# Optimization experiments

Hardware: AMD Instinct MI355X
Metric: run time of the kernel (lower is better)

Reference implementation:

```python
import jax, jax.numpy as jnp
import numpy as np

N = 200_000
E = 3_200_000
H = 24

def setup_inputs() -> dict:
    key = jax.random.key(0)
    ks = jax.random.split(key, 12)
    s = 1.0 / np.sqrt(H).astype(np.float32)
    u = lambda k, shape: jax.random.uniform(k, shape, jnp.float32, -s, s)
    return {
        "x": jax.random.normal(ks[0], (N,), jnp.float32),
        "h0": jax.random.normal(ks[1], (1, N, H), jnp.float32) * 0.1,
        "c0": jax.random.normal(ks[2], (1, N, H), jnp.float32) * 0.1,
        "edge_index": jax.random.randint(ks[3], (2, E), 0, N, dtype=jnp.int32),
        "w_ih": u(ks[4], (4 * H, 1)),
        "w_hh": u(ks[5], (4 * H, H)),
        "b_ih": u(ks[6], (4 * H,)),
        "b_hh": u(ks[7], (4 * H,)),
        "gcn_w": u(ks[8], (H, H)),
        "gcn_b": u(ks[9], (H,)),
        "lin_w": u(ks[10], (1, H)),
        "lin_b": u(ks[11], (1,)),
    }

def reference(x, h0, c0, edge_index, w_ih, w_hh, b_ih, b_hh, gcn_w, gcn_b, lin_w, lin_b):
    # --- LSTM single step (seq_len=1, batch=N, input_size=1, hidden=H) ---
    h_prev = h0[0]  # [N, H]
    c_prev = c0[0]  # [N, H]
    # gates in torch order: input, forget, cell(g), output
    gates = x[:, None] * w_ih[:, 0][None, :] + b_ih + h_prev @ w_hh.T + b_hh  # [N, 4H]
    i, f, g, o = jnp.split(gates, 4, axis=-1)
    i = jax.nn.sigmoid(i); f = jax.nn.sigmoid(f); o = jax.nn.sigmoid(o); g = jnp.tanh(g)
    c = f * c_prev + i * g
    h = o * jnp.tanh(c)  # [N, H] -- LSTM output == new hidden state

    # --- GCNConv(24,24): symmetric norm with self loops (PyG default) ---
    xw = h @ gcn_w.T  # [N, H]
    src, dst = edge_index[0], edge_index[1]
    deg = jax.ops.segment_sum(jnp.ones(src.shape, xw.dtype), dst, num_segments=N) + 1.0
    dinv = jax.lax.rsqrt(deg)                      # deg >= 1 due to self loops
    norm = dinv[src] * dinv[dst]                   # [E]
    msg = xw[src] * norm[:, None]                  # [E, H]
    agg = jax.ops.segment_sum(msg, dst, num_segments=N)
    agg = agg + xw * (dinv * dinv)[:, None]        # self-loop edges
    conv = agg + gcn_b                             # [N, H]

    # --- Linear(24,1) + elementwise gate ---
    out = (conv @ lin_w.T + lin_b).reshape(-1)     # [N]
    return x * out, h[None], c[None]
```

## Files before the change

kernel.cpp:

```cpp
#include <hip/hip_runtime.h>
#include <math.h>

#define H 24
#define B0 4096
#define B0_SHIFT 12
#define MAXNB 64
#define NBPAD 65
#define REP1 8
#define REP3 4
#define P 8
#define CAP 70000
#define CSTRIDE 16
#define K1_EPB 8192
#define EPT (K1_EPB / 256)

__device__ __forceinline__ float sigmoidf_(float v) {
    return 1.0f / (1.0f + __expf(-v));
}
__device__ __forceinline__ float tanhf_(float v) {
    return 1.0f - 2.0f / (__expf(2.0f * v) + 1.0f);
}

__global__ void init_kernel(unsigned* __restrict__ cursors,
                            const float* __restrict__ gcn_w,
                            const float* __restrict__ gcn_b,
                            const float* __restrict__ lin_w,
                            const float* __restrict__ lin_b,
                            float* __restrict__ g, float* __restrict__ cb, int NB) {
    int t = threadIdx.x;
    if (t < H) {
        float acc = 0.0f;
        for (int j = 0; j < H; j++) acc = fmaf(lin_w[j], gcn_w[j * H + t], acc);
        g[t] = acc;
    }
    if (t == 32) {
        float c = lin_b[0];
        for (int j = 0; j < H; j++) c = fmaf(gcn_b[j], lin_w[j], c);
        *cb = c;
    }
    if (t < MAXNB) cursors[t * CSTRIDE] = (unsigned)t * CAP;
}

__global__ __launch_bounds__(256) void scatter_kernel(
    const int* __restrict__ src, const int* __restrict__ dst,
    unsigned* __restrict__ cursors, unsigned* __restrict__ pedge, int E, int NB)
{
    __shared__ unsigned cnt[REP1 * NBPAD];
    __shared__ unsigned rbase[REP3][MAXNB];
    __shared__ unsigned c3[REP3 * NBPAD];
    int start = blockIdx.x * K1_EPB;
    int end   = start + K1_EPB; if (end > E) end = E;
    int rep1 = threadIdx.x & (REP1 - 1);
    int rep3 = rep1 >> 1;

    for (int i = threadIdx.x; i < REP1 * NBPAD; i += 256) cnt[i] = 0;
    __syncthreads();

    unsigned dreg[EPT];
    #pragma unroll
    for (int q = 0; q < EPT; q++) {
        int e = start + q * 256 + threadIdx.x;
        if (e < end) {
            unsigned d = (unsigned)dst[e];
            dreg[q] = d;
            atomicAdd(&cnt[rep1 * NBPAD + (d >> B0_SHIFT)], 1u);
        }
    }
    __syncthreads();

    for (int i = threadIdx.x; i < NB; i += 256) {
        unsigned c[REP1];
        unsigned tot = 0;
        #pragma unroll
        for (int r = 0; r < REP1; r++) { c[r] = cnt[r * NBPAD + i]; tot += c[r]; }
        unsigned gb = tot ? atomicAdd(&cursors[i * CSTRIDE], tot) : 0u;
        unsigned s0 = c[0] + c[1], s1 = c[2] + c[3], s2 = c[4] + c[5];
        rbase[0][i] = gb;
        rbase[1][i] = gb + s0;
        rbase[2][i] = gb + s0 + s1;
        rbase[3][i] = gb + s0 + s1 + s2;
        #pragma unroll
        for (int r = 0; r < REP3; r++) c3[r * NBPAD + i] = 0;
    }
    __syncthreads();

    #pragma unroll
    for (int q = 0; q < EPT; q++) {
        int e = start + q * 256 + threadIdx.x;
        if (e < end) {
            unsigned d = dreg[q];
            unsigned b = d >> B0_SHIFT;
            unsigned slot = atomicAdd(&c3[rep3 * NBPAD + b], 1u);
            unsigned idx  = rbase[rep3][b] + slot;
            if (idx < (b + 1u) * CAP)
                pedge[idx] = ((unsigned)src[e] << B0_SHIFT) | (d & (B0 - 1));
        }
    }
}

__global__ __launch_bounds__(256) void deghist_kernel(
    const unsigned* __restrict__ pedge, const unsigned* __restrict__ cursors,
    unsigned short* __restrict__ degp, int NB, int NPAD)
{
    __shared__ unsigned h[B0];
    int b = blockIdx.x % NB, p = blockIdx.x / NB;
    for (int i = threadIdx.x; i < B0; i += 256) h[i] = 0;
    __syncthreads();
    unsigned base = (unsigned)b * CAP;
    unsigned sz = cursors[b * CSTRIDE] - base; if (sz > CAP) sz = CAP;
    unsigned chunk = (sz + P - 1) / P;
    unsigned s0 = p * chunk;
    unsigned s1 = s0 + chunk; if (s1 > sz) s1 = sz;
    for (unsigned i = s0 + threadIdx.x; i < s1; i += 256)
        atomicAdd(&h[pedge[base + i] & (B0 - 1)], 1u);
    __syncthreads();
    unsigned short* out = degp + (size_t)p * NPAD + (size_t)b * B0;
    for (int i = threadIdx.x; i < B0; i += 256) out[i] = (unsigned short)h[i];
}

__global__ __launch_bounds__(256) void node_kernel(
    const float* __restrict__ x, const float* __restrict__ h0, const float* __restrict__ c0,
    const float* __restrict__ w_ih, const float* __restrict__ w_hh,
    const float* __restrict__ b_ih, const float* __restrict__ b_hh,
    const float* __restrict__ g,
    float* __restrict__ out_h, float* __restrict__ out_c,
    float* __restrict__ y, int N)
{
    __shared__ float ws[96 * 24];
    __shared__ float swih[96];
    __shared__ float sbs[96];
    __shared__ float sg[24];

    #pragma unroll 3
    for (int i = threadIdx.x; i < 96 * 24; i += 256) ws[i] = w_hh[i];
    if (threadIdx.x < 96) {
        swih[threadIdx.x] = w_ih[threadIdx.x];
        sbs[threadIdx.x]  = b_ih[threadIdx.x] + b_hh[threadIdx.x];
    } else if (threadIdx.x >= 128 && threadIdx.x < 152) {
        sg[threadIdx.x - 128] = g[threadIdx.x - 128];
    }
    __syncthreads();

    int tid = blockIdx.x * 256 + threadIdx.x;
    int pr  = tid >> 2;
    int n0  = pr * 2;
    if (n0 >= N) return;
    int n1  = n0 + 1;
    int t   = tid & 3;
    int k0  = 6 * t;

    float hp0[H], hp1[H];
    {
        const float4* a4 = (const float4*)(h0 + (size_t)n0 * H);
        const float4* b4 = (const float4*)(h0 + (size_t)n1 * H);
        #pragma unroll
        for (int q = 0; q < 6; q++) {
            float4 va = a4[q], vb = b4[q];
            hp0[4*q+0] = va.x; hp0[4*q+1] = va.y; hp0[4*q+2] = va.z; hp0[4*q+3] = va.w;
            hp1[4*q+0] = vb.x; hp1[4*q+1] = vb.y; hp1[4*q+2] = vb.z; hp1[4*q+3] = vb.w;
        }
    }
    float cp0[6], cp1[6];
    {
        const float2* a2 = (const float2*)(c0 + (size_t)n0 * H + k0);
        const float2* b2 = (const float2*)(c0 + (size_t)n1 * H + k0);
        #pragma unroll
        for (int q = 0; q < 3; q++) {
            float2 va = a2[q], vb = b2[q];
            cp0[2*q] = va.x; cp0[2*q+1] = va.y;
            cp1[2*q] = vb.x; cp1[2*q+1] = vb.y;
        }
    }
    float xv0 = x[n0], xv1 = x[n1];
    float yv0 = 0.0f, yv1 = 0.0f;

    #pragma unroll
    for (int i = 0; i < 6; i++) {
        int k = k0 + i;
        float bi = sbs[k], bf = sbs[k + 24], bg = sbs[k + 48], bo = sbs[k + 72];
        float wik = swih[k], wfk = swih[k + 24], wgk = swih[k + 48], wok = swih[k + 72];
        float gi0 = fmaf(xv0, wik, bi), gi1 = fmaf(xv1, wik, bi);
        float gf0 = fmaf(xv0, wfk, bf), gf1 = fmaf(xv1, wfk, bf);
        float gg0 = fmaf(xv0, wgk, bg), gg1 = fmaf(xv1, wgk, bg);
        float go0 = fmaf(xv0, wok, bo), go1 = fmaf(xv1, wok, bo);
        const float* w0 = ws + k * 24;
        #pragma unroll
        for (int c = 0; c < 6; c++) {
            float4 wi = *(const float4*)(w0 + 4*c);
            float4 wf = *(const float4*)(w0 + 576  + 4*c);
            float4 wg = *(const float4*)(w0 + 1152 + 4*c);
            float4 wo = *(const float4*)(w0 + 1728 + 4*c);
            float a0 = hp0[4*c+0], a1 = hp0[4*c+1], a2 = hp0[4*c+2], a3 = hp0[4*c+3];
            float d0 = hp1[4*c+0], d1 = hp1[4*c+1], d2 = hp1[4*c+2], d3 = hp1[4*c+3];
            gi0 = fmaf(a0, wi.x, gi0); gi0 = fmaf(a1, wi.y, gi0);
            gi0 = fmaf(a2, wi.z, gi0); gi0 = fmaf(a3, wi.w, gi0);
            gi1 = fmaf(d0, wi.x, gi1); gi1 = fmaf(d1, wi.y, gi1);
            gi1 = fmaf(d2, wi.z, gi1); gi1 = fmaf(d3, wi.w, gi1);
            gf0 = fmaf(a0, wf.x, gf0); gf0 = fmaf(a1, wf.y, gf0);
            gf0 = fmaf(a2, wf.z, gf0); gf0 = fmaf(a3, wf.w, gf0);
            gf1 = fmaf(d0, wf.x, gf1); gf1 = fmaf(d1, wf.y, gf1);
            gf1 = fmaf(d2, wf.z, gf1); gf1 = fmaf(d3, wf.w, gf1);
            gg0 = fmaf(a0, wg.x, gg0); gg0 = fmaf(a1, wg.y, gg0);
            gg0 = fmaf(a2, wg.z, gg0); gg0 = fmaf(a3, wg.w, gg0);
            gg1 = fmaf(d0, wg.x, gg1); gg1 = fmaf(d1, wg.y, gg1);
            gg1 = fmaf(d2, wg.z, gg1); gg1 = fmaf(d3, wg.w, gg1);
            go0 = fmaf(a0, wo.x, go0); go0 = fmaf(a1, wo.y, go0);
            go0 = fmaf(a2, wo.z, go0); go0 = fmaf(a3, wo.w, go0);
            go1 = fmaf(d0, wo.x, go1); go1 = fmaf(d1, wo.y, go1);
            go1 = fmaf(d2, wo.z, go1); go1 = fmaf(d3, wo.w, go1);
        }
        gi0 = sigmoidf_(gi0); gf0 = sigmoidf_(gf0); go0 = sigmoidf_(go0); gg0 = tanhf_(gg0);
        gi1 = sigmoidf_(gi1); gf1 = sigmoidf_(gf1); go1 = sigmoidf_(go1); gg1 = tanhf_(gg1);
        float c_0 = fmaf(gf0, cp0[i], gi0 * gg0);
        float c_1 = fmaf(gf1, cp1[i], gi1 * gg1);
        float h_0 = go0 * tanhf_(c_0);
        float h_1 = go1 * tanhf_(c_1);
        out_c[(size_t)n0 * H + k] = c_0;
        out_c[(size_t)n1 * H + k] = c_1;
        out_h[(size_t)n0 * H + k] = h_0;
        out_h[(size_t)n1 * H + k] = h_1;
        float gk = sg[k];
        yv0 = fmaf(h_0, gk, yv0);
        yv1 = fmaf(h_1, gk, yv1);
    }
    yv0 += __shfl_xor(yv0, 1); yv0 += __shfl_xor(yv0, 2);
    yv1 += __shfl_xor(yv1, 1); yv1 += __shfl_xor(yv1, 2);
    if (t == 0) y[n0] = yv0;
    if (t == 1) y[n1] = yv1;
}

__global__ __launch_bounds__(256) void z_kernel(
    const float* __restrict__ y, const unsigned short* __restrict__ degp, int NPAD,
    float* __restrict__ dinv, float* __restrict__ z, int N)
{
    int n = blockIdx.x * 256 + threadIdx.x;
    if (n >= N) return;
    unsigned dg = 0;
    #pragma unroll
    for (int p = 0; p < P; p++) dg += degp[(size_t)p * NPAD + n];
    float di = rsqrtf((float)dg + 1.0f);
    dinv[n] = di;
    z[n] = di * y[n];
}

__global__ __launch_bounds__(256) void acchist_kernel(
    const unsigned* __restrict__ pedge, const unsigned* __restrict__ cursors,
    const float* __restrict__ z, float* __restrict__ accp, int NB, int NPAD)
{
    __shared__ float h[B0];
    int b = blockIdx.x % NB, p = blockIdx.x / NB;
    for (int i = threadIdx.x; i < B0; i += 256) h[i] = 0.0f;
    __syncthreads();
    unsigned base = (unsigned)b * CAP;
    unsigned sz = cursors[b * CSTRIDE] - base; if (sz > CAP) sz = CAP;
    unsigned chunk = (sz + P - 1) / P;
    unsigned s0 = p * chunk;
    unsigned s1 = s0 + chunk; if (s1 > sz) s1 = sz;
    for (unsigned i = s0 + threadIdx.x; i < s1; i += 256) {
        unsigned v = pedge[base + i];
        atomicAdd(&h[v & (B0 - 1)], z[v >> B0_SHIFT]);
    }
    __syncthreads();
    float* out = accp + (size_t)p * NPAD + (size_t)b * B0;
    for (int i = threadIdx.x; i < B0; i += 256) out[i] = h[i];
}

__global__ __launch_bounds__(256) void final_kernel(
    const float* __restrict__ x, const float* __restrict__ accp, int NPAD,
    const float* __restrict__ y, const float* __restrict__ dinv,
    const float* __restrict__ cb, float* __restrict__ out, int N)
{
    int n = blockIdx.x * blockDim.x + threadIdx.x;
    if (n >= N) return;
    float a = 0.0f;
    #pragma unroll
    for (int p = 0; p < P; p++) a += accp[(size_t)p * NPAD + n];
    float di = dinv[n];
    float s  = di * a + di * di * y[n] + cb[0];
    out[n] = x[n] * s;
}

extern "C" void kernel_launch(void* const* d_in, const int* in_sizes, int n_in,
                              void* d_out, int out_size, void* d_ws, size_t ws_size,
                              hipStream_t stream) {
    const float* x     = (const float*)d_in[0];
    const float* h0    = (const float*)d_in[1];
    const float* c0    = (const float*)d_in[2];
    const int*   ei    = (const int*)d_in[3];
    const float* w_ih  = (const float*)d_in[4];
    const float* w_hh  = (const float*)d_in[5];
    const float* b_ih  = (const float*)d_in[6];
    const float* b_hh  = (const float*)d_in[7];
    const float* gcn_w = (const float*)d_in[8];
    const float* gcn_b = (const float*)d_in[9];
    const float* lin_w = (const float*)d_in[10];
    const float* lin_b = (const float*)d_in[11];

    const int N = in_sizes[0];
    const int E = in_sizes[3] / 2;
    const int* src = ei;
    const int* dst = ei + E;

    const int NB   = (N + B0 - 1) / B0;
    const int NPAD = NB * B0;

    float* out_gate = (float*)d_out;
    float* out_h    = out_gate + N;
    float* out_c    = out_h + (size_t)N * H;

    char* w = (char*)d_ws;
    unsigned*       pedge   = (unsigned*)w;       w += (size_t)NB * CAP * 4;
    unsigned short* degp    = (unsigned short*)w; w += (size_t)P * NPAD * 2;
    float*          accp    = (float*)w;          w += (size_t)P * NPAD * 4;
    float*          y       = (float*)w;          w += (size_t)N * 4;
    float*          zv      = (float*)w;          w += (size_t)N * 4;
    float*          dinv    = (float*)w;          w += (size_t)N * 4;
    float*          g       = (float*)w;          w += H * 4;
    float*          cb      = (float*)w;          w += 4;
    unsigned*       cursors = (unsigned*)w;       w += MAXNB * CSTRIDE * 4;

    init_kernel   <<<1, 64, 0, stream>>>(cursors, gcn_w, gcn_b, lin_w, lin_b, g, cb, NB);
    scatter_kernel<<<(E + K1_EPB - 1) / K1_EPB, 256, 0, stream>>>(src, dst, cursors,
                                                                  pedge, E, NB);
    deghist_kernel<<<NB * P, 256, 0, stream>>>(pedge, cursors, degp, NB, NPAD);
    node_kernel   <<<((size_t)N * 2 + 255) / 256, 256, 0, stream>>>(
                       x, h0, c0, w_ih, w_hh, b_ih, b_hh, g, out_h, out_c, y, N);
    z_kernel      <<<(N + 255) / 256, 256, 0, stream>>>(y, degp, NPAD, dinv, zv, N);
    acchist_kernel<<<NB * P, 256, 0, stream>>>(pedge, cursors, zv, accp, NB, NPAD);
    final_kernel  <<<(N + 255) / 256, 256, 0, stream>>>(x, accp, NPAD, y, dinv, cb,
                                                        out_gate, N);
}
```

Measured before the change: 119.3 us.

## Restructure edge scatter: per-wave histograms, vectorized 16-edge-per-thread loads, smaller blocks

The bucket-scatter kernel now gives each thread 16 contiguous edges loaded as uint4 vectors instead of strided scalar loads. It keeps one shared-memory histogram per wavefront rather than eight interleaved replicas, and halves the edges per block so more blocks run. Src indices are prefetched into registers with vector loads before the write phase. The cost is that edges within a wave are no longer interleaved across threads, so writes to pedge are less coalesced and shared atomics are more likely to hit the same counter within a wave.

```diff
diff --git a/kernel.cpp b/kernel.cpp
--- a/kernel.cpp
+++ b/kernel.cpp
@@ -6,13 +6,10 @@
 #define B0_SHIFT 12
 #define MAXNB 64
 #define NBPAD 65
-#define REP1 8
-#define REP3 4
 #define P 8
 #define CAP 70000
 #define CSTRIDE 16
-#define K1_EPB 8192
-#define EPT (K1_EPB / 256)
+#define K1_EPB 4096
 
 __device__ __forceinline__ float sigmoidf_(float v) {
     return 1.0f / (1.0f + __expf(-v));
@@ -45,55 +42,86 @@
     const int* __restrict__ src, const int* __restrict__ dst,
     unsigned* __restrict__ cursors, unsigned* __restrict__ pedge, int E, int NB)
 {
-    __shared__ unsigned cnt[REP1 * NBPAD];
-    __shared__ unsigned rbase[REP3][MAXNB];
-    __shared__ unsigned c3[REP3 * NBPAD];
-    int start = blockIdx.x * K1_EPB;
-    int end   = start + K1_EPB; if (end > E) end = E;
-    int rep1 = threadIdx.x & (REP1 - 1);
-    int rep3 = rep1 >> 1;
-
-    for (int i = threadIdx.x; i < REP1 * NBPAD; i += 256) cnt[i] = 0;
-    __syncthreads();
-
-    unsigned dreg[EPT];
-    #pragma unroll
-    for (int q = 0; q < EPT; q++) {
-        int e = start + q * 256 + threadIdx.x;
-        if (e < end) {
-            unsigned d = (unsigned)dst[e];
-            dreg[q] = d;
-            atomicAdd(&cnt[rep1 * NBPAD + (d >> B0_SHIFT)], 1u);
-        }
-    }
-    __syncthreads();
-
-    for (int i = threadIdx.x; i < NB; i += 256) {
-        unsigned c[REP1];
-        unsigned tot = 0;
-        #pragma unroll
-        for (int r = 0; r < REP1; r++) { c[r] = cnt[r * NBPAD + i]; tot += c[r]; }
-        unsigned gb = tot ? atomicAdd(&cursors[i * CSTRIDE], tot) : 0u;
-        unsigned s0 = c[0] + c[1], s1 = c[2] + c[3], s2 = c[4] + c[5];
-        rbase[0][i] = gb;
-        rbase[1][i] = gb + s0;
-        rbase[2][i] = gb + s0 + s1;
-        rbase[3][i] = gb + s0 + s1 + s2;
-        #pragma unroll
-        for (int r = 0; r < REP3; r++) c3[r * NBPAD + i] = 0;
-    }
-    __syncthreads();
-
-    #pragma unroll
-    for (int q = 0; q < EPT; q++) {
-        int e = start + q * 256 + threadIdx.x;
-        if (e < end) {
+    __shared__ unsigned cnt[4][NBPAD];
+    __shared__ unsigned c3[4][NBPAD];
+    __shared__ unsigned base[4][NBPAD];
+
+    const int tid = threadIdx.x;
+    const int w = tid >> 6;
+    const int start = blockIdx.x * K1_EPB;
+    const bool full = (E - start) >= K1_EPB;
+    const int ebase = start + tid * 16;
+
+    for (int i = tid; i < 4 * NBPAD; i += 256) {
+        (&cnt[0][0])[i] = 0;
+        (&c3[0][0])[i] = 0;
+    }
+    __syncthreads();
+
+    unsigned dreg[16];
+    if (full) {
+        const uint4* dp = (const uint4*)(dst + ebase);
+        #pragma unroll
+        for (int q = 0; q < 4; q++) {
+            uint4 v = dp[q];
+            dreg[4*q+0] = v.x; dreg[4*q+1] = v.y; dreg[4*q+2] = v.z; dreg[4*q+3] = v.w;
+        }
+        #pragma unroll
+        for (int q = 0; q < 16; q++)
+            atomicAdd(&cnt[w][dreg[q] >> B0_SHIFT], 1u);
+    } else {
+        #pragma unroll
+        for (int q = 0; q < 16; q++) {
+            int e = ebase + q;
+            if (e < E) {
+                unsigned d = (unsigned)dst[e];
+                dreg[q] = d;
+                atomicAdd(&cnt[w][d >> B0_SHIFT], 1u);
+            } else dreg[q] = 0xFFFFFFFFu;
+        }
+    }
+    __syncthreads();
+
+    if (tid < NB) {
+        unsigned c0 = cnt[0][tid], c1 = cnt[1][tid], c2 = cnt[2][tid], cw3 = cnt[3][tid];
+        unsigned tot = c0 + c1 + c2 + cw3;
+        unsigned gb = tot ? atomicAdd(&cursors[tid * CSTRIDE], tot) : 0u;
+        base[0][tid] = gb;
+        base[1][tid] = gb + c0;
+        base[2][tid] = gb + c0 + c1;
+        base[3][tid] = gb + c0 + c1 + c2;
+    }
+    __syncthreads();
+
+    if (full) {
+        unsigned sreg[16];
+        const uint4* sp = (const uint4*)(src + ebase);
+        #pragma unroll
+        for (int q = 0; q < 4; q++) {
+            uint4 v = sp[q];
+            sreg[4*q+0] = v.x; sreg[4*q+1] = v.y; sreg[4*q+2] = v.z; sreg[4*q+3] = v.w;
+        }
+        #pragma unroll
+        for (int q = 0; q < 16; q++) {
             unsigned d = dreg[q];
             unsigned b = d >> B0_SHIFT;
-            unsigned slot = atomicAdd(&c3[rep3 * NBPAD + b], 1u);
-            unsigned idx  = rbase[rep3][b] + slot;
+            unsigned slot = atomicAdd(&c3[w][b], 1u);
+            unsigned idx  = base[w][b] + slot;
             if (idx < (b + 1u) * CAP)
-                pedge[idx] = ((unsigned)src[e] << B0_SHIFT) | (d & (B0 - 1));
+                pedge[idx] = (sreg[q] << B0_SHIFT) | (d & (B0 - 1));
+        }
+    } else {
+        #pragma unroll
+        for (int q = 0; q < 16; q++) {
+            int e = ebase + q;
+            if (e < E) {
+                unsigned d = dreg[q];
+                unsigned b = d >> B0_SHIFT;
+                unsigned slot = atomicAdd(&c3[w][b], 1u);
+                unsigned idx  = base[w][b] + slot;
+                if (idx < (b + 1u) * CAP)
+                    pedge[idx] = ((unsigned)src[e] << B0_SHIFT) | (d & (B0 - 1));
+            }
         }
     }
 }
```

Result: faster. 113.6 us (-4.8%).
